# Kernel optimization log

Hardware: AMD Instinct MI355X
Metric: run time of the kernel (lower is better)

## Reference

```python
import jax, jax.numpy as jnp
import numpy as np

N = 50000
E = 600000
D = 128


def gcn_conv(x, row, col, w, W, b):
    """PyG GCNConv: add self-loops (weight 1), symmetric deg^-1/2 normalization,
    linear transform, edge-weighted scatter-add aggregation, then bias."""
    n = x.shape[0]
    loop = jnp.arange(n)
    r = jnp.concatenate([row, loop])            # source nodes, [E+N]
    c = jnp.concatenate([col, loop])            # target nodes, [E+N]
    ww = jnp.concatenate([w, jnp.ones((n,), x.dtype)])
    deg = jax.ops.segment_sum(ww, c, num_segments=n)          # weighted in-degree
    dinv = jnp.where(deg > 0, jax.lax.rsqrt(deg), jnp.zeros_like(deg))
    norm = dinv[r] * ww * dinv[c]               # [E+N]
    xl = x @ W                                  # [n, D_out]
    msg = norm[:, None] * xl[r]                 # gather + scale, [E+N, D_out]
    out = jax.ops.segment_sum(msg, c, num_segments=n)
    return out + b


def setup_inputs() -> dict:
    key = jax.random.key(0)
    ks = jax.random.split(key, 12)
    x = jax.random.normal(ks[0], (N, D), dtype=jnp.float32)
    edge_index = jax.random.randint(ks[1], (2, E), 0, N, dtype=jnp.int64)
    edge_weights = jax.random.uniform(ks[2], (E,), dtype=jnp.float32)
    s = 1.0 / np.sqrt(D)
    W1 = jax.random.uniform(ks[3], (D, D), jnp.float32, -s, s)
    b1 = jnp.zeros((D,), jnp.float32)
    W2 = jax.random.uniform(ks[4], (D, D), jnp.float32, -s, s)
    b2 = jnp.zeros((D,), jnp.float32)
    W3 = jax.random.uniform(ks[5], (D, D), jnp.float32, -s, s)
    b3 = jnp.zeros((D,), jnp.float32)
    prelu_w = jnp.array(0.25, jnp.float32)
    return {"x": x, "edge_index": edge_index, "edge_weights": edge_weights,
            "W1": W1, "b1": b1, "W2": W2, "b2": b2, "W3": W3, "b3": b3,
            "prelu_w": prelu_w}


def reference(x, edge_index, edge_weights, W1, b1, W2, b2, W3, b3, prelu_w):
    row, col = edge_index[0], edge_index[1]
    # layer 1: GCNConv -> (dropout: eval, identity) -> ELU
    h = gcn_conv(x, row, col, edge_weights, W1, b1)
    h = jax.nn.elu(h)
    # layer 2: GCNConv -> GELU (torch default = exact erf)
    h = gcn_conv(h, row, col, edge_weights, W2, b2)
    h = jax.nn.gelu(h, approximate=False)
    # layer 3: GCNConv -> PReLU (learnable scalar slope)
    h = gcn_conv(h, row, col, edge_weights, W3, b3)
    h = jnp.where(h >= 0, h, prelu_w * h)
    return h
```

## Files before the change

kernel.cpp:

```cpp
#include <hip/hip_runtime.h>
#include <hip/hip_fp16.h>
#include <math.h>

constexpr int D = 128;

struct __align__(16) H8 { __half2 h[4]; };
struct __align__(8)  H4 { __half2 a, b; };

typedef _Float16 half8 __attribute__((ext_vector_type(8)));
typedef float    floatx4 __attribute__((ext_vector_type(4)));


__device__ __forceinline__ int detect64(const int* __restrict__ ei) {
  int z = 0;
#pragma unroll
  for (int i = 0; i < 8; ++i) z |= ei[2 * i + 1];
  return (z == 0) ? 1 : 0;
}

__device__ __forceinline__ void load_edge(const int* __restrict__ ei, int e, int nE,
                                          int m64, int n, int& r, int& c) {
  if (m64) { r = ei[2 * (size_t)e]; c = ei[2 * ((size_t)nE + e)]; }
  else     { r = ei[(size_t)e];     c = ei[(size_t)nE + e]; }
  r = min(max(r, 0), n - 1);
  c = min(max(c, 0), n - 1);
}

__global__ void k_zero(int* __restrict__ cnt, int n) {
  int i = blockIdx.x * blockDim.x + threadIdx.x;
  if (i < n) cnt[i] = 0;
}

__global__ void k_pos(const int* __restrict__ ei, int* __restrict__ cnt,
                      int2* __restrict__ rc, int* __restrict__ pos, int nE, int n) {
  int e = blockIdx.x * blockDim.x + threadIdx.x;
  if (e >= nE) return;
  int m64 = detect64(ei);
  int r, c;
  load_edge(ei, e, nE, m64, n, r, c);
  rc[e] = make_int2(r, c);
  pos[e] = atomicAdd(&cnt[c], 1);
}

__global__ void k_scan1(const int* __restrict__ cnt, int* __restrict__ offs,
                        int* __restrict__ bsum, int n) {
  __shared__ int s[256];
  int t = threadIdx.x;
  int i = blockIdx.x * 256 + t;
  int v = (i < n) ? cnt[i] : 0;
  s[t] = v;
  __syncthreads();
  for (int off = 1; off < 256; off <<= 1) {
    int x = 0;
    if (t >= off) x = s[t - off];
    __syncthreads();
    if (t >= off) s[t] += x;
    __syncthreads();
  }
  if (i < n) offs[i] = s[t] - v;
  if (t == 255) bsum[blockIdx.x] = s[255];
}

__global__ void k_scan2(const int* __restrict__ bsum, int* __restrict__ boff, int nb) {
  __shared__ int s[256];
  int t = threadIdx.x;
  int v = (t < nb) ? bsum[t] : 0;
  s[t] = v;
  __syncthreads();
  for (int off = 1; off < 256; off <<= 1) {
    int x = 0;
    if (t >= off) x = s[t - off];
    __syncthreads();
    if (t >= off) s[t] += x;
    __syncthreads();
  }
  if (t < nb) boff[t] = s[t] - v;
}

__global__ void k_scan3(int* __restrict__ offs, const int* __restrict__ boff, int n, int nE) {
  int i = blockIdx.x * 256 + threadIdx.x;
  if (i < n) offs[i] += boff[blockIdx.x];
  if (i == 0) offs[n] = nE;
}

__global__ void k_fill(const int2* __restrict__ rc, const int* __restrict__ pos,
                       const float* __restrict__ w, const int* __restrict__ offs,
                       int2* __restrict__ ecf, int nE) {
  int e = blockIdx.x * blockDim.x + threadIdx.x;
  if (e >= nE) return;
  int2 p = rc[e];
  int idx = offs[p.y] + pos[e];
  ecf[idx] = make_int2(p.x, __float_as_int(w[e]));
}

__global__ void k_degdinv(const int2* __restrict__ ecf, const int* __restrict__ offs,
                          float* __restrict__ dinv, int n) {
  int i = blockIdx.x * blockDim.x + threadIdx.x;
  if (i >= n) return;
  float s = 1.0f;
  int e1 = offs[i + 1];
  for (int e = offs[i]; e < e1; ++e) s += __int_as_float(ecf[e].y);
  dinv[i] = rsqrtf(s);
}

__global__ void k_coef(const int2* __restrict__ ecf, const float* __restrict__ dinv,
                       unsigned int* __restrict__ ecf2, int nE) {
  int e = blockIdx.x * blockDim.x + threadIdx.x;
  if (e >= nE) return;
  int2 p = ecf[e];
  float c = dinv[p.x] * __int_as_float(p.y);
  ecf2[e] = ((unsigned int)p.x << 16) |
            (unsigned int)__half_as_ushort(__float2half_rn(c));
}

__global__ void k_wt(const float* __restrict__ W1, const float* __restrict__ W2,
                     const float* __restrict__ W3, __half* __restrict__ Wt) {
  __shared__ float s[128][129];
  const float* W = blockIdx.x == 0 ? W1 : (blockIdx.x == 1 ? W2 : W3);
  __half* o = Wt + (size_t)blockIdx.x * D * D;
  int tid = threadIdx.x;
#pragma unroll
  for (int i = 0; i < 16; ++i) {
    int flat = i * 1024 + tid * 4;
    int k = flat >> 7;
    int nn = flat & 127;
    float4 v = *(const float4*)(W + (size_t)k * D + nn);
    s[k][nn] = v.x; s[k][nn + 1] = v.y; s[k][nn + 2] = v.z; s[k][nn + 3] = v.w;
  }
  __syncthreads();
#pragma unroll
  for (int i = 0; i < 8; ++i) {
    int flat = i * 256 + tid;
    int nn = flat >> 4;
    int k0 = (flat & 15) * 8;
    H8 hv;
#pragma unroll
    for (int t = 0; t < 4; ++t)
      hv.h[t] = __floats2half2_rn(s[k0 + 2 * t][nn], s[k0 + 2 * t + 1][nn]);
    *(H8*)(o + (size_t)nn * D + k0) = hv;
  }
}

template <int ACT>
__device__ __forceinline__ float act_f(float x) {
  if (ACT == 1) return x > 0.f ? x : expm1f(x);
  if (ACT == 2) return 0.5f * x * (1.0f + erff(x * 0.70710678118654752440f));
  return x;
}

template <int ACT, typename AT>
__global__ __launch_bounds__(256) void k_gemm(const AT* __restrict__ A,
                                              const __half* __restrict__ Wt,
                                              __half* __restrict__ Y, int n) {
  const int wave = threadIdx.x >> 6;
  const int lane = threadIdx.x & 63;
  const int np = lane & 15;
  const int quad = lane >> 4;
  const int node = blockIdx.x * 64 + wave * 16 + np;
  const int nc = min(node, n - 1);

  half8 b[4];
#pragma unroll
  for (int s = 0; s < 4; ++s) {
    if constexpr (sizeof(AT) == 4) {
      const float* ap = (const float*)A + (size_t)nc * D + s * 32 + quad * 8;
      float4 v0 = *(const float4*)ap;
      float4 v1 = *(const float4*)(ap + 4);
      b[s][0] = (_Float16)act_f<ACT>(v0.x); b[s][1] = (_Float16)act_f<ACT>(v0.y);
      b[s][2] = (_Float16)act_f<ACT>(v0.z); b[s][3] = (_Float16)act_f<ACT>(v0.w);
      b[s][4] = (_Float16)act_f<ACT>(v1.x); b[s][5] = (_Float16)act_f<ACT>(v1.y);
      b[s][6] = (_Float16)act_f<ACT>(v1.z); b[s][7] = (_Float16)act_f<ACT>(v1.w);
    } else {
      half8 raw = *(const half8*)((const __half*)A + ((size_t)s * n + nc) * 32 + quad * 8);
#pragma unroll
      for (int t = 0; t < 8; ++t)
        b[s][t] = (_Float16)act_f<ACT>((float)raw[t]);
    }
  }

  floatx4 acc[8];
#pragma unroll
  for (int mt = 0; mt < 8; ++mt) acc[mt] = (floatx4){0.f, 0.f, 0.f, 0.f};

#pragma unroll
  for (int mt = 0; mt < 8; ++mt) {
#pragma unroll
    for (int s = 0; s < 4; ++s) {
      half8 a = *(const half8*)(Wt + (size_t)(mt * 16 + np) * D + s * 32 + quad * 8);
      acc[mt] = __builtin_amdgcn_mfma_f32_16x16x32_f16(a, b[s], acc[mt], 0, 0, 0);
    }
  }

  if (node < n) {
#pragma unroll
    for (int mt = 0; mt < 8; ++mt) {
      H4 hv;
      hv.a = __floats2half2_rn(acc[mt][0], acc[mt][1]);
      hv.b = __floats2half2_rn(acc[mt][2], acc[mt][3]);
      int f0 = mt * 16 + quad * 4;
      *(H4*)(Y + ((size_t)(f0 >> 5) * n + node) * 32 + (f0 & 31)) = hv;
    }
  }
}

__device__ __forceinline__ void fmacc8(float* acc, float c, const H8& y) {
  float2 f;
  f = __half22float2(y.h[0]); acc[0] += c * f.x; acc[1] += c * f.y;
  f = __half22float2(y.h[1]); acc[2] += c * f.x; acc[3] += c * f.y;
  f = __half22float2(y.h[2]); acc[4] += c * f.x; acc[5] += c * f.y;
  f = __half22float2(y.h[3]); acc[6] += c * f.x; acc[7] += c * f.y;
}

__device__ __forceinline__ float cdecode(unsigned int u) {
  return __half2float(__ushort_as_half((unsigned short)(u & 0xffffu)));
}

template <int PRELU, typename OutT>
__global__ __launch_bounds__(256) void k_agg(const __half* __restrict__ Y,
                                             const int* __restrict__ offs,
                                             const unsigned int* __restrict__ ecf2,
                                             const float* __restrict__ dinv,
                                             const float* __restrict__ bias,
                                             const float* __restrict__ pw,
                                             OutT* __restrict__ OUT, int n) {
  const int chunk = blockIdx.x & 3;
  const int t = threadIdx.x;
  const int node = (blockIdx.x >> 2) * 32 + (t >> 3);
  const int sub = (t >> 2) & 1;
  const int j = t & 3;
  if (node >= n) return;
  const __half* Yc = Y + (size_t)chunk * n * 32;
  float dc = dinv[node];
  float acc[8] = {0.f, 0.f, 0.f, 0.f, 0.f, 0.f, 0.f, 0.f};
  if (sub == 0) {
    H8 ys = *(const H8*)(Yc + (size_t)node * 32 + j * 8);
    fmacc8(acc, dc, ys);
  }
  int e0 = offs[node], e1 = offs[node + 1];
  int e = e0 + sub;
  for (; e + 6 < e1; e += 8) {
    unsigned int u0 = ecf2[e], u1 = ecf2[e + 2], u2 = ecf2[e + 4], u3 = ecf2[e + 6];
    H8 y0 = *(const H8*)(Yc + (size_t)(u0 >> 16) * 32 + j * 8);
    H8 y1 = *(const H8*)(Yc + (size_t)(u1 >> 16) * 32 + j * 8);
    H8 y2 = *(const H8*)(Yc + (size_t)(u2 >> 16) * 32 + j * 8);
    H8 y3 = *(const H8*)(Yc + (size_t)(u3 >> 16) * 32 + j * 8);
    fmacc8(acc, cdecode(u0), y0);
    fmacc8(acc, cdecode(u1), y1);
    fmacc8(acc, cdecode(u2), y2);
    fmacc8(acc, cdecode(u3), y3);
  }
  for (; e < e1; e += 2) {
    unsigned int u = ecf2[e];
    H8 y = *(const H8*)(Yc + (size_t)(u >> 16) * 32 + j * 8);
    fmacc8(acc, cdecode(u), y);
  }
#pragma unroll
  for (int i = 0; i < 8; ++i) acc[i] += __shfl_xor(acc[i], 4, 64);
  float4 b4 = *(const float4*)(bias + chunk * 32 + j * 8 + sub * 4);
  float o[4];
  o[0] = dc * acc[sub * 4 + 0] + b4.x;
  o[1] = dc * acc[sub * 4 + 1] + b4.y;
  o[2] = dc * acc[sub * 4 + 2] + b4.z;
  o[3] = dc * acc[sub * 4 + 3] + b4.w;
  if (PRELU) {
    float wv = *pw;
#pragma unroll
    for (int i = 0; i < 4; ++i) o[i] = o[i] >= 0.f ? o[i] : wv * o[i];
  }
  if constexpr (sizeof(OutT) == 4) {
    *(float4*)((float*)OUT + (size_t)node * D + chunk * 32 + j * 8 + sub * 4) =
        make_float4(o[0], o[1], o[2], o[3]);
  } else {
    H4 hv;
    hv.a = __floats2half2_rn(o[0], o[1]);
    hv.b = __floats2half2_rn(o[2], o[3]);
    *(H4*)((__half*)OUT + ((size_t)chunk * n + node) * 32 + j * 8 + sub * 4) = hv;
  }
}

extern "C" void kernel_launch(void* const* d_in, const int* in_sizes, int n_in,
                              void* d_out, int out_size, void* d_ws, size_t ws_size,
                              hipStream_t stream) {
  const float* x  = (const float*)d_in[0];
  const int*   ei = (const int*)d_in[1];
  const float* w  = (const float*)d_in[2];
  const float* W1 = (const float*)d_in[3];
  const float* b1 = (const float*)d_in[4];
  const float* W2 = (const float*)d_in[5];
  const float* b2 = (const float*)d_in[6];
  const float* W3 = (const float*)d_in[7];
  const float* b3 = (const float*)d_in[8];
  const float* pw = (const float*)d_in[9];
  const int N = in_sizes[0] / D;
  const int E = in_sizes[2];
  float* out = (float*)d_out;

  char* wsb = (char*)d_ws;
  size_t off = 0;
  auto alloc = [&](size_t bytes) {
    void* p = wsb + off;
    off = (off + bytes + 255) & ~(size_t)255;
    return p;
  };
  float*        dinv = (float*)alloc((size_t)N * 4);
  int*          cnt  = (int*)alloc((size_t)N * 4);
  int*          offs = (int*)alloc((size_t)(N + 1) * 4);
  int*          bsum = (int*)alloc(256 * 4);
  int*          boff = (int*)alloc(256 * 4);
  int2*         ecf  = (int2*)alloc((size_t)E * 8);
  unsigned int* ecf2 = (unsigned int*)alloc((size_t)E * 4);
  __half*       Wt   = (__half*)alloc((size_t)3 * D * D * 2);
  __half*       Y    = (__half*)alloc((size_t)N * D * 2);
  __half*       h    = (__half*)alloc((size_t)N * D * 2);
  int2*         rc   = (int2*)Y;
  int*          pos  = (int*)((char*)Y + (size_t)E * 8);

  const int nb = (N + 255) / 256;
  const int eb = (E + 255) / 256;

  hipLaunchKernelGGL(k_wt,      dim3(3),  dim3(256), 0, stream, W1, W2, W3, Wt);
  hipLaunchKernelGGL(k_zero,    dim3(nb), dim3(256), 0, stream, cnt, N);
  hipLaunchKernelGGL(k_pos,     dim3(eb), dim3(256), 0, stream, ei, cnt, rc, pos, E, N);
  hipLaunchKernelGGL(k_scan1,   dim3(nb), dim3(256), 0, stream, cnt, offs, bsum, N);
  hipLaunchKernelGGL(k_scan2,   dim3(1),  dim3(256), 0, stream, bsum, boff, nb);
  hipLaunchKernelGGL(k_scan3,   dim3(nb), dim3(256), 0, stream, offs, boff, N, E);
  hipLaunchKernelGGL(k_fill,    dim3(eb), dim3(256), 0, stream, rc, pos, w, offs, ecf, E);
  hipLaunchKernelGGL(k_degdinv, dim3(nb), dim3(256), 0, stream, ecf, offs, dinv, N);
  hipLaunchKernelGGL(k_coef,    dim3(eb), dim3(256), 0, stream, ecf, dinv, ecf2, E);

  const int gb = (N + 63) / 64;
  const int ab = 4 * ((N + 31) / 32);

  hipLaunchKernelGGL((k_gemm<0, float>),  dim3(gb), dim3(256), 0, stream, x, Wt,             Y, N);
  hipLaunchKernelGGL((k_agg<0, __half>),  dim3(ab), dim3(256), 0, stream, Y, offs, ecf2, dinv, b1, pw, h, N);
  hipLaunchKernelGGL((k_gemm<1, __half>), dim3(gb), dim3(256), 0, stream, h, Wt + D * D,     Y, N);
  hipLaunchKernelGGL((k_agg<0, __half>),  dim3(ab), dim3(256), 0, stream, Y, offs, ecf2, dinv, b2, pw, h, N);
  hipLaunchKernelGGL((k_gemm<2, __half>), dim3(gb), dim3(256), 0, stream, h, Wt + 2 * D * D, Y, N);
  hipLaunchKernelGGL((k_agg<1, float>),   dim3(ab), dim3(256), 0, stream, Y, offs, ecf2, dinv, b3, pw, out, N);
}
```

Baseline: 299.6 us.

## Fuse CSR preprocessing kernels, pad rows to 4, vectorize edge loads, nontemporal I/O

Several preprocessing kernels are merged: the weight transpose and zeroing become one launch, the degree is accumulated with float atomics during counting, dinv is computed in the scan fixup, and edge coefficients are written directly during CSR fill. The kernel count drops and the separate degree and coefficient passes over the edges go away. CSR rows are padded to multiples of 4 with zero entries so the aggregation can load four packed edges with one 128-bit load and split each row into halves. Nontemporal loads and stores are added in the GEMM and aggregation kernels. Float atomics make the degree sum order nondeterministic, and padding adds memory and some wasted gathers of row 0.

```diff
diff --git a/kernel.cpp b/kernel.cpp
--- a/kernel.cpp
+++ b/kernel.cpp
@@ -5,10 +5,11 @@
 constexpr int D = 128;
 
 struct __align__(16) H8 { __half2 h[4]; };
-struct __align__(8)  H4 { __half2 a, b; };
-
-typedef _Float16 half8 __attribute__((ext_vector_type(8)));
-typedef float    floatx4 __attribute__((ext_vector_type(4)));
+
+typedef _Float16     half8   __attribute__((ext_vector_type(8)));
+typedef float        floatx4 __attribute__((ext_vector_type(4)));
+typedef unsigned int uint4v  __attribute__((ext_vector_type(4)));
+typedef unsigned int uint2v  __attribute__((ext_vector_type(2)));
 
 
 __device__ __forceinline__ int detect64(const int* __restrict__ ei) {
@@ -26,12 +27,34 @@
   c = min(max(c, 0), n - 1);
 }
 
-__global__ void k_zero(int* __restrict__ cnt, int n) {
-  int i = blockIdx.x * blockDim.x + threadIdx.x;
-  if (i < n) cnt[i] = 0;
-}
-
-__global__ void k_pos(const int* __restrict__ ei, int* __restrict__ cnt,
+__global__ void k_setup(const float* __restrict__ W1, const float* __restrict__ W2,
+                        const float* __restrict__ W3, __half* __restrict__ Wt,
+                        int* __restrict__ cnt, float* __restrict__ deg, int n) {
+  int b = blockIdx.x;
+  if (b < 24) {
+    int m = b >> 3, s = b & 7;
+    const float* W = m == 0 ? W1 : (m == 1 ? W2 : W3);
+    __half* o = Wt + (size_t)m * D * D;
+    int t = threadIdx.x;
+    int nn = t & 127;
+    int kh = t >> 7;
+    int k0 = s * 16 + kh * 8;
+    H8 hv;
+#pragma unroll
+    for (int jj = 0; jj < 4; ++jj) {
+      float f0 = W[(size_t)(k0 + 2 * jj)     * D + nn];
+      float f1 = W[(size_t)(k0 + 2 * jj + 1) * D + nn];
+      hv.h[jj] = __floats2half2_rn(f0, f1);
+    }
+    *(H8*)(o + (size_t)nn * D + k0) = hv;
+  } else {
+    int i = (b - 24) * 256 + threadIdx.x;
+    if (i < n) { cnt[i] = 0; deg[i] = 0.f; }
+  }
+}
+
+__global__ void k_pos(const int* __restrict__ ei, const float* __restrict__ w,
+                      int* __restrict__ cnt, float* __restrict__ deg,
                       int2* __restrict__ rc, int* __restrict__ pos, int nE, int n) {
   int e = blockIdx.x * blockDim.x + threadIdx.x;
   if (e >= nE) return;
@@ -40,6 +63,7 @@
   load_edge(ei, e, nE, m64, n, r, c);
   rc[e] = make_int2(r, c);
   pos[e] = atomicAdd(&cnt[c], 1);
+  atomicAdd(&deg[c], w[e]);
 }
 
 __global__ void k_scan1(const int* __restrict__ cnt, int* __restrict__ offs,
@@ -47,7 +71,7 @@
   __shared__ int s[256];
   int t = threadIdx.x;
   int i = blockIdx.x * 256 + t;
-  int v = (i < n) ? cnt[i] : 0;
+  int v = (i < n) ? ((cnt[i] + 3) & ~3) : 0;
   s[t] = v;
   __syncthreads();
   for (int off = 1; off < 256; off <<= 1) {
@@ -77,67 +101,32 @@
   if (t < nb) boff[t] = s[t] - v;
 }
 
-__global__ void k_scan3(int* __restrict__ offs, const int* __restrict__ boff, int n, int nE) {
+__global__ void k_scan3(int* __restrict__ offs, const int* __restrict__ boff,
+                        const int* __restrict__ bsum, const float* __restrict__ deg,
+                        float* __restrict__ dinv, int n, int nb) {
   int i = blockIdx.x * 256 + threadIdx.x;
-  if (i < n) offs[i] += boff[blockIdx.x];
-  if (i == 0) offs[n] = nE;
+  if (i < n) {
+    offs[i] += boff[blockIdx.x];
+    dinv[i] = rsqrtf(1.0f + deg[i]);
+  }
+  if (i == 0) offs[n] = boff[nb - 1] + bsum[nb - 1];
 }
 
 __global__ void k_fill(const int2* __restrict__ rc, const int* __restrict__ pos,
                        const float* __restrict__ w, const int* __restrict__ offs,
-                       int2* __restrict__ ecf, int nE) {
+                       const int* __restrict__ cnt, const float* __restrict__ dinv,
+                       unsigned int* __restrict__ ecf2, int nE, int n) {
   int e = blockIdx.x * blockDim.x + threadIdx.x;
-  if (e >= nE) return;
-  int2 p = rc[e];
-  int idx = offs[p.y] + pos[e];
-  ecf[idx] = make_int2(p.x, __float_as_int(w[e]));
-}
-
-__global__ void k_degdinv(const int2* __restrict__ ecf, const int* __restrict__ offs,
-                          float* __restrict__ dinv, int n) {
-  int i = blockIdx.x * blockDim.x + threadIdx.x;
-  if (i >= n) return;
-  float s = 1.0f;
-  int e1 = offs[i + 1];
-  for (int e = offs[i]; e < e1; ++e) s += __int_as_float(ecf[e].y);
-  dinv[i] = rsqrtf(s);
-}
-
-__global__ void k_coef(const int2* __restrict__ ecf, const float* __restrict__ dinv,
-                       unsigned int* __restrict__ ecf2, int nE) {
-  int e = blockIdx.x * blockDim.x + threadIdx.x;
-  if (e >= nE) return;
-  int2 p = ecf[e];
-  float c = dinv[p.x] * __int_as_float(p.y);
-  ecf2[e] = ((unsigned int)p.x << 16) |
-            (unsigned int)__half_as_ushort(__float2half_rn(c));
-}
-
-__global__ void k_wt(const float* __restrict__ W1, const float* __restrict__ W2,
-                     const float* __restrict__ W3, __half* __restrict__ Wt) {
-  __shared__ float s[128][129];
-  const float* W = blockIdx.x == 0 ? W1 : (blockIdx.x == 1 ? W2 : W3);
-  __half* o = Wt + (size_t)blockIdx.x * D * D;
-  int tid = threadIdx.x;
-#pragma unroll
-  for (int i = 0; i < 16; ++i) {
-    int flat = i * 1024 + tid * 4;
-    int k = flat >> 7;
-    int nn = flat & 127;
-    float4 v = *(const float4*)(W + (size_t)k * D + nn);
-    s[k][nn] = v.x; s[k][nn + 1] = v.y; s[k][nn + 2] = v.z; s[k][nn + 3] = v.w;
-  }
-  __syncthreads();
-#pragma unroll
-  for (int i = 0; i < 8; ++i) {
-    int flat = i * 256 + tid;
-    int nn = flat >> 4;
-    int k0 = (flat & 15) * 8;
-    H8 hv;
-#pragma unroll
-    for (int t = 0; t < 4; ++t)
-      hv.h[t] = __floats2half2_rn(s[k0 + 2 * t][nn], s[k0 + 2 * t + 1][nn]);
-    *(H8*)(o + (size_t)nn * D + k0) = hv;
+  if (e < nE) {
+    int2 p = rc[e];
+    int idx = offs[p.y] + pos[e];
+    float cf = dinv[p.x] * w[e];
+    ecf2[idx] = ((unsigned int)p.x << 16) |
+                (unsigned int)__half_as_ushort(__float2half_rn(cf));
+  }
+  if (e < n) {
+    int q0 = offs[e] + cnt[e], q1 = offs[e + 1];
+    for (int q = q0; q < q1; ++q) ecf2[q] = 0;
   }
 }
 
@@ -164,14 +153,16 @@
   for (int s = 0; s < 4; ++s) {
     if constexpr (sizeof(AT) == 4) {
       const float* ap = (const float*)A + (size_t)nc * D + s * 32 + quad * 8;
-      float4 v0 = *(const float4*)ap;
-      float4 v1 = *(const float4*)(ap + 4);
-      b[s][0] = (_Float16)act_f<ACT>(v0.x); b[s][1] = (_Float16)act_f<ACT>(v0.y);
-      b[s][2] = (_Float16)act_f<ACT>(v0.z); b[s][3] = (_Float16)act_f<ACT>(v0.w);
-      b[s][4] = (_Float16)act_f<ACT>(v1.x); b[s][5] = (_Float16)act_f<ACT>(v1.y);
-      b[s][6] = (_Float16)act_f<ACT>(v1.z); b[s][7] = (_Float16)act_f<ACT>(v1.w);
+      floatx4 v0 = __builtin_nontemporal_load((const floatx4*)ap);
+      floatx4 v1 = __builtin_nontemporal_load((const floatx4*)(ap + 4));
+#pragma unroll
+      for (int t = 0; t < 4; ++t) {
+        b[s][t]     = (_Float16)act_f<ACT>(v0[t]);
+        b[s][t + 4] = (_Float16)act_f<ACT>(v1[t]);
+      }
     } else {
-      half8 raw = *(const half8*)((const __half*)A + ((size_t)s * n + nc) * 32 + quad * 8);
+      half8 raw = __builtin_nontemporal_load(
+          (const half8*)((const __half*)A + ((size_t)s * n + nc) * 32 + quad * 8));
 #pragma unroll
       for (int t = 0; t < 8; ++t)
         b[s][t] = (_Float16)act_f<ACT>((float)raw[t]);
@@ -194,21 +185,22 @@
   if (node < n) {
 #pragma unroll
     for (int mt = 0; mt < 8; ++mt) {
-      H4 hv;
-      hv.a = __floats2half2_rn(acc[mt][0], acc[mt][1]);
-      hv.b = __floats2half2_rn(acc[mt][2], acc[mt][3]);
+      __half2 ha = __floats2half2_rn(acc[mt][0], acc[mt][1]);
+      __half2 hb = __floats2half2_rn(acc[mt][2], acc[mt][3]);
+      uint2v pv;
+      pv[0] = *(unsigned int*)&ha;
+      pv[1] = *(unsigned int*)&hb;
       int f0 = mt * 16 + quad * 4;
-      *(H4*)(Y + ((size_t)(f0 >> 5) * n + node) * 32 + (f0 & 31)) = hv;
+      __builtin_nontemporal_store(
+          pv, (uint2v*)(Y + ((size_t)(f0 >> 5) * n + node) * 32 + (f0 & 31)));
     }
   }
 }
 
 __device__ __forceinline__ void fmacc8(float* acc, float c, const H8& y) {
-  float2 f;
-  f = __half22float2(y.h[0]); acc[0] += c * f.x; acc[1] += c * f.y;
-  f = __half22float2(y.h[1]); acc[2] += c * f.x; acc[3] += c * f.y;
-  f = __half22float2(y.h[2]); acc[4] += c * f.x; acc[5] += c * f.y;
-  f = __half22float2(y.h[3]); acc[6] += c * f.x; acc[7] += c * f.y;
+  const _Float16* hp = (const _Float16*)&y;
+#pragma unroll
+  for (int i = 0; i < 8; ++i) acc[i] = fmaf(c, (float)hp[i], acc[i]);
 }
 
 __device__ __forceinline__ float cdecode(unsigned int u) {
@@ -236,45 +228,48 @@
     H8 ys = *(const H8*)(Yc + (size_t)node * 32 + j * 8);
     fmacc8(acc, dc, ys);
   }
-  int e0 = offs[node], e1 = offs[node + 1];
-  int e = e0 + sub;
-  for (; e + 6 < e1; e += 8) {
-    unsigned int u0 = ecf2[e], u1 = ecf2[e + 2], u2 = ecf2[e + 4], u3 = ecf2[e + 6];
-    H8 y0 = *(const H8*)(Yc + (size_t)(u0 >> 16) * 32 + j * 8);
-    H8 y1 = *(const H8*)(Yc + (size_t)(u1 >> 16) * 32 + j * 8);
-    H8 y2 = *(const H8*)(Yc + (size_t)(u2 >> 16) * 32 + j * 8);
-    H8 y3 = *(const H8*)(Yc + (size_t)(u3 >> 16) * 32 + j * 8);
-    fmacc8(acc, cdecode(u0), y0);
-    fmacc8(acc, cdecode(u1), y1);
-    fmacc8(acc, cdecode(u2), y2);
-    fmacc8(acc, cdecode(u3), y3);
-  }
-  for (; e < e1; e += 2) {
-    unsigned int u = ecf2[e];
-    H8 y = *(const H8*)(Yc + (size_t)(u >> 16) * 32 + j * 8);
-    fmacc8(acc, cdecode(u), y);
-  }
-#pragma unroll
-  for (int i = 0; i < 8; ++i) acc[i] += __shfl_xor(acc[i], 4, 64);
-  float4 b4 = *(const float4*)(bias + chunk * 32 + j * 8 + sub * 4);
+  int lo = offs[node], hi = offs[node + 1];
+  int nb4 = (hi - lo) >> 2;
+  int em = lo + (((nb4 + 1) >> 1) << 2);
+  int b0 = sub ? em : lo;
+  int b1 = sub ? hi : em;
+  for (int b = b0; b < b1; b += 4) {
+    uint4v u = __builtin_nontemporal_load((const uint4v*)(ecf2 + b));
+    H8 y0 = *(const H8*)(Yc + (size_t)(u[0] >> 16) * 32 + j * 8);
+    H8 y1 = *(const H8*)(Yc + (size_t)(u[1] >> 16) * 32 + j * 8);
+    H8 y2 = *(const H8*)(Yc + (size_t)(u[2] >> 16) * 32 + j * 8);
+    H8 y3 = *(const H8*)(Yc + (size_t)(u[3] >> 16) * 32 + j * 8);
+    fmacc8(acc, cdecode(u[0]), y0);
+    fmacc8(acc, cdecode(u[1]), y1);
+    fmacc8(acc, cdecode(u[2]), y2);
+    fmacc8(acc, cdecode(u[3]), y3);
+  }
+  floatx4 b4 = *(const floatx4*)(bias + chunk * 32 + j * 8 + sub * 4);
   float o[4];
-  o[0] = dc * acc[sub * 4 + 0] + b4.x;
-  o[1] = dc * acc[sub * 4 + 1] + b4.y;
-  o[2] = dc * acc[sub * 4 + 2] + b4.z;
-  o[3] = dc * acc[sub * 4 + 3] + b4.w;
+#pragma unroll
+  for (int i = 0; i < 4; ++i) {
+    float mine  = sub ? acc[4 + i] : acc[i];
+    float other = sub ? acc[i]     : acc[4 + i];
+    float recv = __shfl_xor(other, 4, 64);
+    o[i] = dc * (mine + recv) + b4[i];
+  }
   if (PRELU) {
     float wv = *pw;
 #pragma unroll
     for (int i = 0; i < 4; ++i) o[i] = o[i] >= 0.f ? o[i] : wv * o[i];
   }
   if constexpr (sizeof(OutT) == 4) {
-    *(float4*)((float*)OUT + (size_t)node * D + chunk * 32 + j * 8 + sub * 4) =
-        make_float4(o[0], o[1], o[2], o[3]);
+    floatx4 ov = {o[0], o[1], o[2], o[3]};
+    __builtin_nontemporal_store(
+        ov, (floatx4*)((float*)OUT + (size_t)node * D + chunk * 32 + j * 8 + sub * 4));
   } else {
-    H4 hv;
-    hv.a = __floats2half2_rn(o[0], o[1]);
-    hv.b = __floats2half2_rn(o[2], o[3]);
-    *(H4*)((__half*)OUT + ((size_t)chunk * n + node) * 32 + j * 8 + sub * 4) = hv;
+    __half2 ha = __floats2half2_rn(o[0], o[1]);
+    __half2 hb = __floats2half2_rn(o[2], o[3]);
+    uint2v pv;
+    pv[0] = *(unsigned int*)&ha;
+    pv[1] = *(unsigned int*)&hb;
+    __builtin_nontemporal_store(
+        pv, (uint2v*)((__half*)OUT + ((size_t)chunk * n + node) * 32 + j * 8 + sub * 4));
   }
 }
 
@@ -303,30 +298,28 @@
     return p;
   };
   float*        dinv = (float*)alloc((size_t)N * 4);
+  float*        deg  = (float*)alloc((size_t)N * 4);
   int*          cnt  = (int*)alloc((size_t)N * 4);
   int*          offs = (int*)alloc((size_t)(N + 1) * 4);
   int*          bsum = (int*)alloc(256 * 4);
   int*          boff = (int*)alloc(256 * 4);
-  int2*         ecf  = (int2*)alloc((size_t)E * 8);
-  unsigned int* ecf2 = (unsigned int*)alloc((size_t)E * 4);
+  unsigned int* ecf2 = (unsigned int*)alloc(((size_t)E + 3 * (size_t)N + 64) * 4);
   __half*       Wt   = (__half*)alloc((size_t)3 * D * D * 2);
   __half*       Y    = (__half*)alloc((size_t)N * D * 2);
   __half*       h    = (__half*)alloc((size_t)N * D * 2);
   int2*         rc   = (int2*)Y;
   int*          pos  = (int*)((char*)Y + (size_t)E * 8);
 
-  const int nb = (N + 255) / 256;
-  const int eb = (E + 255) / 256;
-
-  hipLaunchKernelGGL(k_wt,      dim3(3),  dim3(256), 0, stream, W1, W2, W3, Wt);
-  hipLaunchKernelGGL(k_zero,    dim3(nb), dim3(256), 0, stream, cnt, N);
-  hipLaunchKernelGGL(k_pos,     dim3(eb), dim3(256), 0, stream, ei, cnt, rc, pos, E, N);
-  hipLaunchKernelGGL(k_scan1,   dim3(nb), dim3(256), 0, stream, cnt, offs, bsum, N);
-  hipLaunchKernelGGL(k_scan2,   dim3(1),  dim3(256), 0, stream, bsum, boff, nb);
-  hipLaunchKernelGGL(k_scan3,   dim3(nb), dim3(256), 0, stream, offs, boff, N, E);
-  hipLaunchKernelGGL(k_fill,    dim3(eb), dim3(256), 0, stream, rc, pos, w, offs, ecf, E);
-  hipLaunchKernelGGL(k_degdinv, dim3(nb), dim3(256), 0, stream, ecf, offs, dinv, N);
-  hipLaunchKernelGGL(k_coef,    dim3(eb), dim3(256), 0, stream, ecf, dinv, ecf2, E);
+  const int nbN = (N + 255) / 256;
+  const int eb  = (E + 255) / 256;
+  const int fb  = ((E > N ? E : N) + 255) / 256;
+
+  hipLaunchKernelGGL(k_setup, dim3(24 + nbN), dim3(256), 0, stream, W1, W2, W3, Wt, cnt, deg, N);
+  hipLaunchKernelGGL(k_pos,   dim3(eb),  dim3(256), 0, stream, ei, w, cnt, deg, rc, pos, E, N);
+  hipLaunchKernelGGL(k_scan1, dim3(nbN), dim3(256), 0, stream, cnt, offs, bsum, N);
+  hipLaunchKernelGGL(k_scan2, dim3(1),   dim3(256), 0, stream, bsum, boff, nbN);
+  hipLaunchKernelGGL(k_scan3, dim3(nbN), dim3(256), 0, stream, offs, boff, bsum, deg, dinv, N, nbN);
+  hipLaunchKernelGGL(k_fill,  dim3(fb),  dim3(256), 0, stream, rc, pos, w, offs, cnt, dinv, ecf2, E, N);
 
   const int gb = (N + 63) / 64;
   const int ab = 4 * ((N + 31) / 32);
```

Result: slower. 331.1 us (+10.5%).
